# Kernel tuning notes

Measured on AMD Instinct MI355X. Metric: run time of the kernel, lower is better.

Reference implementation:

```python
import jax, jax.numpy as jnp
import numpy as np

N_HEADS = 8
N_DIM = 512
ATTN_DIM = N_DIM // N_HEADS
SOFT_TEMPERATURE = 1.0
TEMPERATURE = ATTN_DIM ** 0.5 / SOFT_TEMPERATURE


def sparsemax(z):
    # sparsemax along last axis: euclidean projection onto the simplex
    n = z.shape[-1]
    z_sorted = -jnp.sort(-z, axis=-1)                      # descending
    cs = jnp.cumsum(z_sorted, axis=-1)
    k = jnp.arange(1, n + 1, dtype=z.dtype)
    support = 1.0 + k * z_sorted > cs                      # bool
    k_sel = jnp.sum(support, axis=-1, keepdims=True)       # support size >= 1
    cs_sel = jnp.take_along_axis(cs, k_sel - 1, axis=-1)
    tau = (cs_sel - 1.0) / k_sel.astype(z.dtype)
    return jnp.maximum(z - tau, 0.0)


def setup_inputs() -> dict:
    key = jax.random.key(0)
    ks = jax.random.split(key, 9)
    bs, L, d = 8, 1024, N_DIM
    s = 1.0 / np.sqrt(d)
    return {
        "h_q": jax.random.normal(ks[0], (bs, L, d), jnp.float32),
        "h_k": jax.random.normal(ks[1], (bs, L, d), jnp.float32),
        "h_v": jax.random.normal(ks[2], (bs, L, d), jnp.float32),
        "Wq": jax.random.normal(ks[3], (d, d), jnp.float32) * s,
        "Wk": jax.random.normal(ks[4], (d, d), jnp.float32) * s,
        "Wv": jax.random.normal(ks[5], (d, d), jnp.float32) * s,
        "bv": jax.random.normal(ks[6], (d,), jnp.float32) * s,
        "Wf": jax.random.normal(ks[7], (d, d), jnp.float32) * s,
        "bf": jax.random.normal(ks[8], (d,), jnp.float32) * s,
    }


def reference(h_q, h_k, h_v, Wq, Wk, Wv, bv, Wf, bf):
    bs, Lq, _ = h_q.shape
    Lk = h_k.shape[1]
    H, D = N_HEADS, ATTN_DIM
    q = (h_q @ Wq.T).reshape(bs, Lq, H, D).transpose(0, 2, 1, 3)   # bhqd
    k = (h_k @ Wk.T).reshape(bs, Lk, H, D).transpose(0, 2, 1, 3)   # bhkd
    v = (h_v @ Wv.T + bv).reshape(bs, Lk, H, D).transpose(0, 2, 1, 3)
    alpha = jnp.einsum('bhqd,bhkd->bhqk', q / TEMPERATURE, k)
    alpha = sparsemax(alpha)
    res = jnp.einsum('bhqk,bhkd->bhqd', alpha, v)
    res = res.transpose(0, 2, 1, 3).reshape(bs, Lq, H * D)
    return res @ Wf.T + bf
```

## Files before the change

kernel.cpp:

```cpp
#include <hip/hip_runtime.h>
#include <hip/hip_bf16.h>
#include <cstdint>
#include <cstddef>

#define BS 8
#define SEQ 1024
#define DMODEL 512
#define NHEADS 8
#define DHEAD 64
#define QBLK 16
#define PPAD 1032

typedef float f32x4 __attribute__((ext_vector_type(4)));
typedef short bf16x8 __attribute__((ext_vector_type(8)));

static __device__ __forceinline__ unsigned short f2bf(float v) {
    __hip_bfloat16 hb = __float2bfloat16(v);
    return *reinterpret_cast<unsigned short*>(&hb);
}

struct CvtJob { const float* s; unsigned short* d; int n4; };

__global__ __launch_bounds__(256) void cvt_many(
    CvtJob j0, CvtJob j1, CvtJob j2, CvtJob j3, CvtJob j4, CvtJob j5, CvtJob j6)
{
    CvtJob j;
    switch (blockIdx.y) {
        case 0: j = j0; break; case 1: j = j1; break; case 2: j = j2; break;
        case 3: j = j3; break; case 4: j = j4; break; case 5: j = j5; break;
        default: j = j6; break;
    }
    for (int i = blockIdx.x * 256 + threadIdx.x; i < j.n4; i += gridDim.x * 256) {
        const float4 f = ((const float4*)j.s)[i];
        uint2 u;
        u.x = (unsigned)f2bf(f.x) | ((unsigned)f2bf(f.y) << 16);
        u.y = (unsigned)f2bf(f.z) | ((unsigned)f2bf(f.w) << 16);
        ((uint2*)j.d)[i] = u;
    }
}

struct GArgs { const unsigned short* A; const unsigned short* W;
               const float* bias; void* C; void* C2; float scale; int mode; };

__global__ __launch_bounds__(256) void gemm_mfma(GArgs g0, GArgs g1, GArgs g2) {
    __shared__ __align__(16) unsigned short As[64 * 64];
    __shared__ __align__(16) unsigned short Bs[128 * 64];

    const GArgs g = (blockIdx.z == 0) ? g0 : ((blockIdx.z == 1) ? g1 : g2);
    const int tid = threadIdx.x;
    const int w = tid >> 6, l = tid & 63, lr = l & 15, lg = l >> 4;
    const int bm = blockIdx.y * 64, bn = blockIdx.x * 128;
    const int mrow = (w & 1) * 32, ncol = (w >> 1) * 64;

    f32x4 acc[2][4];
#pragma unroll
    for (int mt = 0; mt < 2; ++mt)
#pragma unroll
        for (int nt = 0; nt < 4; ++nt) acc[mt][nt] = (f32x4)0.f;

    for (int k0 = 0; k0 < DMODEL; k0 += 64) {
#pragma unroll
        for (int i = 0; i < 2; ++i) {
            const int rbase = i * 32 + w * 8;
            const int r = rbase + (l >> 3);
            const unsigned short* src = g.A + (size_t)(bm + r) * DMODEL + k0
                                        + 8 * ((l & 7) ^ (r & 7));
            __builtin_amdgcn_global_load_lds((const unsigned int*)src,
                                             (unsigned int*)&As[rbase * 64], 16, 0, 0);
        }
#pragma unroll
        for (int i = 0; i < 4; ++i) {
            const int rbase = i * 32 + w * 8;
            const int r = rbase + (l >> 3);
            const unsigned short* src = g.W + (size_t)(bn + r) * DMODEL + k0
                                        + 8 * ((l & 7) ^ (r & 7));
            __builtin_amdgcn_global_load_lds((const unsigned int*)src,
                                             (unsigned int*)&Bs[rbase * 64], 16, 0, 0);
        }
        __syncthreads();
#pragma unroll
        for (int kk = 0; kk < 2; ++kk) {
            bf16x8 av[2], bv[4];
#pragma unroll
            for (int mt = 0; mt < 2; ++mt) {
                const int ra = mrow + mt * 16 + lr;
                av[mt] = *(const bf16x8*)&As[ra * 64 + 8 * ((kk * 4 + lg) ^ (ra & 7))];
            }
#pragma unroll
            for (int nt = 0; nt < 4; ++nt) {
                const int rb = ncol + nt * 16 + lr;
                bv[nt] = *(const bf16x8*)&Bs[rb * 64 + 8 * ((kk * 4 + lg) ^ (rb & 7))];
            }
#pragma unroll
            for (int mt = 0; mt < 2; ++mt)
#pragma unroll
                for (int nt = 0; nt < 4; ++nt)
                    acc[mt][nt] = __builtin_amdgcn_mfma_f32_16x16x32_bf16(
                        av[mt], bv[nt], acc[mt][nt], 0, 0, 0);
        }
        __syncthreads();
    }

    if (g.mode == 0) {
        float* C = (float*)g.C;
#pragma unroll
        for (int mt = 0; mt < 2; ++mt)
#pragma unroll
        for (int nt = 0; nt < 4; ++nt)
#pragma unroll
        for (int j = 0; j < 4; ++j) {
            const int r = bm + mrow + mt * 16 + lg * 4 + j;
            const int c = bn + ncol + nt * 16 + lr;
            C[(size_t)r * DMODEL + c] = acc[mt][nt][j] * g.scale
                                        + (g.bias ? g.bias[c] : 0.f);
        }
    } else {
        if (g.mode == 1 || g.mode == 3) {
            unsigned short* C = (unsigned short*)g.C;
#pragma unroll
            for (int mt = 0; mt < 2; ++mt)
#pragma unroll
            for (int nt = 0; nt < 4; ++nt)
#pragma unroll
            for (int j = 0; j < 4; ++j) {
                const int r = bm + mrow + mt * 16 + lg * 4 + j;
                const int c = bn + ncol + nt * 16 + lr;
                const float v = acc[mt][nt][j] * g.scale + (g.bias ? g.bias[c] : 0.f);
                const int b = r >> 10, ll = r & (SEQ - 1);
                const int h = c >> 6, dd = c & 63;
                C[((size_t)(b * NHEADS + h) * SEQ + ll) * DHEAD + dd] = f2bf(v);
            }
        }
        if (g.mode == 2 || g.mode == 3) {
            unsigned short* C = (unsigned short*)((g.mode == 3) ? g.C2 : g.C);
#pragma unroll
            for (int mt = 0; mt < 2; ++mt)
#pragma unroll
            for (int nt = 0; nt < 4; ++nt) {
                const int c = bn + ncol + nt * 16 + lr;
                const int h = c >> 6, dd = c & 63;
                const int r0 = bm + mrow + mt * 16 + lg * 4;
                const int b = r0 >> 10, l0 = r0 & (SEQ - 1);
                unsigned short tmp[4];
#pragma unroll
                for (int j = 0; j < 4; ++j)
                    tmp[j] = f2bf(acc[mt][nt][j] * g.scale + (g.bias ? g.bias[c] : 0.f));
                uint2 u;
                u.x = (unsigned)tmp[0] | ((unsigned)tmp[1] << 16);
                u.y = (unsigned)tmp[2] | ((unsigned)tmp[3] << 16);
                *(uint2*)&C[((size_t)(b * NHEADS + h) * DHEAD + dd) * SEQ + l0] = u;
            }
        }
    }
}

__global__ __launch_bounds__(256, 3) void attn_mfma(
    const unsigned short* __restrict__ Q, const unsigned short* __restrict__ K,
    const unsigned short* __restrict__ Vt, const unsigned short* __restrict__ Vn,
    unsigned short* __restrict__ R)
{
    __shared__ __align__(16) unsigned char pool[33024];
    __shared__ __align__(16) float clist[QBLK][66];
    __shared__ __align__(16) unsigned short cidx[QBLK][66];
    __shared__ int cnt_s[QBLK];
    __shared__ __align__(16) float red_m[QBLK][4];
    __shared__ __align__(16) float red_s[2][QBLK][4];
    __shared__ __align__(16) float red_c[2][QBLK][4];
    __shared__ float tau_s[QBLK];

    unsigned short* Ks = (unsigned short*)pool;
    unsigned short (*P)[PPAD] = (unsigned short (*)[PPAD])pool;

    const int tid = threadIdx.x;
    const int w = tid >> 6, l = tid & 63, lr = l & 15, lg = l >> 4;

    const int flat = blockIdx.x;
    const int nid = (flat & 7) * 512 + (flat >> 3);
    const int q0 = (nid & 63) * QBLK;
    const int h = (nid >> 6) & (NHEADS - 1);
    const int b = nid >> 9;

    const size_t base = (size_t)(b * NHEADS + h) * SEQ * DHEAD;
    const unsigned short* Qp = Q + base;
    const unsigned short* Kp = K + base;

    const bf16x8 aq0 = *(const bf16x8*)(Qp + (size_t)(q0 + lr) * DHEAD + lg * 8);
    const bf16x8 aq1 = *(const bf16x8*)(Qp + (size_t)(q0 + lr) * DHEAD + 32 + lg * 8);

#define STAGE(CH, BUF)                                                         \
    {                                                                          \
        _Pragma("unroll")                                                      \
        for (int i = 0; i < 4; ++i) {                                          \
            const int rbase = i * 32 + w * 8;                                  \
            const int r = rbase + (l >> 3);                                    \
            const unsigned short* src = Kp + (size_t)((CH) * 128 + r) * DHEAD  \
                                        + 8 * ((l & 7) ^ (r & 7));             \
            __builtin_amdgcn_global_load_lds((const unsigned int*)src,         \
                (unsigned int*)&Ks[(BUF) * 8192 + rbase * 64], 16, 0, 0);      \
        }                                                                      \
    }

    f32x4 acc[16];
#pragma unroll
    for (int a = 0; a < 16; ++a) acc[a] = (f32x4)0.f;

    STAGE(0, 0)
    __syncthreads();
#pragma unroll
    for (int c = 0; c < 8; ++c) {
        const int buf = c & 1;
        if (c + 1 < 8) STAGE(c + 1, buf ^ 1)
        const unsigned short* kb = Ks + buf * 8192;
#pragma unroll
        for (int tt = 0; tt < 2; ++tt) {
            const int ra = w * 32 + tt * 16 + lr;
            const bf16x8 k0 = *(const bf16x8*)&kb[ra * 64 + 8 * ((0 + lg) ^ (ra & 7))];
            const bf16x8 k1 = *(const bf16x8*)&kb[ra * 64 + 8 * ((4 + lg) ^ (ra & 7))];
            acc[2 * c + tt] = __builtin_amdgcn_mfma_f32_16x16x32_bf16(
                k0, aq0, acc[2 * c + tt], 0, 0, 0);
            acc[2 * c + tt] = __builtin_amdgcn_mfma_f32_16x16x32_bf16(
                k1, aq1, acc[2 * c + tt], 0, 0, 0);
        }
        __syncthreads();
    }
#undef STAGE

    f32x4 m4 = acc[0];
#pragma unroll
    for (int a = 1; a < 16; ++a) {
        m4[0] = fmaxf(m4[0], acc[a][0]); m4[1] = fmaxf(m4[1], acc[a][1]);
        m4[2] = fmaxf(m4[2], acc[a][2]); m4[3] = fmaxf(m4[3], acc[a][3]);
    }
    float m = fmaxf(fmaxf(m4[0], m4[1]), fmaxf(m4[2], m4[3]));
    m = fmaxf(m, __shfl_xor(m, 16));
    m = fmaxf(m, __shfl_xor(m, 32));
    if (lg == 0) red_m[lr][w] = m;

    for (int i = tid; i < QBLK * 66; i += 256) (&clist[0][0])[i] = -3.0e38f;
    if (tid < QBLK) cnt_s[tid] = 0;
    __syncthreads();

    const float4 rm4 = *(const float4*)red_m[lr];
    const float rmax = fmaxf(fmaxf(rm4.x, rm4.y), fmaxf(rm4.z, rm4.w));
    float tau = rmax - 1.0f;
    const float thr = tau;

#pragma unroll
    for (int a = 0; a < 16; ++a)
#pragma unroll
        for (int j = 0; j < 4; ++j) {
            const float z = acc[a][j];
            if (z > thr) {
                const int pos = atomicAdd(&cnt_s[lr], 1);
                if (pos < 64) {
                    clist[lr][pos] = z;
                    cidx[lr][pos] = (unsigned short)((a >> 1) * 128 + w * 32
                                                     + (a & 1) * 16 + lg * 4 + j);
                }
            }
        }
    __syncthreads();

    const bool anyfull = __any(cnt_s[lr] > 64);

    if (!anyfull) {
        const f32x4* clp = (const f32x4*)&clist[lr][lg * 16];
        const f32x4 cd0 = clp[0], cd1 = clp[1], cd2 = clp[2], cd3 = clp[3];
        for (int it = 0; it < 16; ++it) {
            float s = 0.f, c = 0.f;
#pragma unroll
            for (int i = 0; i < 4; ++i) {
                const float z0 = cd0[i], z1 = cd1[i], z2 = cd2[i], z3 = cd3[i];
                if (z0 > tau) { s += z0; c += 1.f; }
                if (z1 > tau) { s += z1; c += 1.f; }
                if (z2 > tau) { s += z2; c += 1.f; }
                if (z3 > tau) { s += z3; c += 1.f; }
            }
            s += __shfl_xor(s, 16); c += __shfl_xor(c, 16);
            s += __shfl_xor(s, 32); c += __shfl_xor(c, 32);
            const float tn = (s - 1.f) / c;
            float delta = tn - tau;
            tau = tn;
            delta = fmaxf(delta, __shfl_xor(delta, 1));
            delta = fmaxf(delta, __shfl_xor(delta, 2));
            delta = fmaxf(delta, __shfl_xor(delta, 4));
            delta = fmaxf(delta, __shfl_xor(delta, 8));
            if (delta < 1e-5f) break;
        }
        if (w == 0 && lg == 0) tau_s[lr] = tau;
        __syncthreads();

        const int r = tid >> 4;
        const int dt = tid & 15;
        const float taur = tau_s[r];
        const int cntc = cnt_s[r];
        const unsigned short* Vrow = Vn + base + dt * 4;
        f32x4 o = (f32x4)0.f;
        float z0, z1, z2, z3;
        uint2 v0, v1, v2, v3;
#define SLOAD(ZS, VS, I)                                                       \
    {                                                                          \
        const int ii = (I) < cntc ? (I) : 0;                                   \
        ZS = clist[r][ii];                                                     \
        VS = *(const uint2*)(Vrow + (size_t)cidx[r][ii] * DHEAD);              \
    }
#define SMAC(ZS, VS)                                                           \
    {                                                                          \
        const float wgt = fmaxf(ZS - taur, 0.f);                               \
        o[0] += wgt * __uint_as_float(VS.x << 16);                             \
        o[1] += wgt * __uint_as_float(VS.x & 0xffff0000u);                     \
        o[2] += wgt * __uint_as_float(VS.y << 16);                             \
        o[3] += wgt * __uint_as_float(VS.y & 0xffff0000u);                     \
    }
        SLOAD(z0, v0, 0) SLOAD(z1, v1, 1) SLOAD(z2, v2, 2) SLOAD(z3, v3, 3)
        for (int i = 0; i < cntc; i += 4) {
            SMAC(z0, v0)
            if (i + 1 < cntc) SMAC(z1, v1)
            if (i + 2 < cntc) SMAC(z2, v2)
            if (i + 3 < cntc) SMAC(z3, v3)
            SLOAD(z0, v0, i + 4) SLOAD(z1, v1, i + 5)
            SLOAD(z2, v2, i + 6) SLOAD(z3, v3, i + 7)
        }
#undef SLOAD
#undef SMAC
        unsigned short t4[4];
#pragma unroll
        for (int j = 0; j < 4; ++j) t4[j] = f2bf(o[j]);
        uint2 u;
        u.x = (unsigned)t4[0] | ((unsigned)t4[1] << 16);
        u.y = (unsigned)t4[2] | ((unsigned)t4[3] << 16);
        *(uint2*)&R[((size_t)b * SEQ + q0 + r) * DMODEL + h * DHEAD + dt * 4] = u;
        return;
    }

    for (int it = 0; it < 16; ++it) {
        const int bb = (it + 1) & 1;
        float s = 0.f, c = 0.f;
#pragma unroll
        for (int a = 0; a < 16; ++a)
#pragma unroll
            for (int j = 0; j < 4; ++j) {
                const float z = acc[a][j];
                if (z > tau) { s += z; c += 1.f; }
            }
        s += __shfl_xor(s, 16); c += __shfl_xor(c, 16);
        s += __shfl_xor(s, 32); c += __shfl_xor(c, 32);
        if (lg == 0) { red_s[bb][lr][w] = s; red_c[bb][lr][w] = c; }
        __syncthreads();
        const float4 s4 = *(const float4*)red_s[bb][lr];
        const float4 c4 = *(const float4*)red_c[bb][lr];
        const float st = (s4.x + s4.y) + (s4.z + s4.w);
        const float ct = (c4.x + c4.y) + (c4.z + c4.w);
        const float tn = (st - 1.f) / ct;
        float delta = tn - tau;
        tau = tn;
        delta = fmaxf(delta, __shfl_xor(delta, 1));
        delta = fmaxf(delta, __shfl_xor(delta, 2));
        delta = fmaxf(delta, __shfl_xor(delta, 4));
        delta = fmaxf(delta, __shfl_xor(delta, 8));
        if (delta < 1e-5f) break;
    }
    __syncthreads();

#pragma unroll
    for (int a = 0; a < 16; ++a)
#pragma unroll
        for (int jp = 0; jp < 2; ++jp) {
            const unsigned lo = f2bf(fmaxf(acc[a][2 * jp] - tau, 0.f));
            const unsigned hi = f2bf(fmaxf(acc[a][2 * jp + 1] - tau, 0.f));
            const int key = (a >> 1) * 128 + w * 32 + (a & 1) * 16 + lg * 4 + 2 * jp;
            *(unsigned*)&P[lr][key] = lo | (hi << 16);
        }
    __syncthreads();

    const int dcol = w * 16;
    const unsigned short* VtP = Vt + ((size_t)(b * NHEADS + h) * DHEAD + dcol + lr) * SEQ
                                + lg * 8;
    f32x4 o = (f32x4)0.f;
    bf16x8 vb0 = *(const bf16x8*)(VtP + 0 * 32);
    bf16x8 vb1 = *(const bf16x8*)(VtP + 1 * 32);
    bf16x8 vb2 = *(const bf16x8*)(VtP + 2 * 32);
    bf16x8 vb3 = *(const bf16x8*)(VtP + 3 * 32);
#define PV_STEP(KT, VREG)                                                      \
    {                                                                          \
        const bf16x8 pa = *(const bf16x8*)&P[lr][(KT) * 32 + lg * 8];          \
        o = __builtin_amdgcn_mfma_f32_16x16x32_bf16(pa, VREG, o, 0, 0, 0);     \
        if ((KT) + 4 < 32) VREG = *(const bf16x8*)(VtP + ((KT) + 4) * 32);     \
    }
    for (int kt = 0; kt < 32; kt += 4) {
        PV_STEP(kt + 0, vb0)
        PV_STEP(kt + 1, vb1)
        PV_STEP(kt + 2, vb2)
        PV_STEP(kt + 3, vb3)
    }
#undef PV_STEP

#pragma unroll
    for (int j = 0; j < 4; ++j)
        R[((size_t)b * SEQ + q0 + lg * 4 + j) * DMODEL + h * DHEAD + dcol + lr] =
            f2bf(o[j]);
}

extern "C" void kernel_launch(void* const* d_in, const int* in_sizes, int n_in,
                              void* d_out, int out_size, void* d_ws, size_t ws_size,
                              hipStream_t stream) {
    const float* h_q = (const float*)d_in[0];
    const float* h_k = (const float*)d_in[1];
    const float* h_v = (const float*)d_in[2];
    const float* Wq  = (const float*)d_in[3];
    const float* Wk  = (const float*)d_in[4];
    const float* Wv  = (const float*)d_in[5];
    const float* bv  = (const float*)d_in[6];
    const float* Wf  = (const float*)d_in[7];
    const float* bf  = (const float*)d_in[8];
    float* out = (float*)d_out;

    const size_t perT = (size_t)BS * SEQ * DMODEL;
    const size_t wN = (size_t)DMODEL * DMODEL;
    unsigned short* hq_b = (unsigned short*)d_ws;
    unsigned short* hk_b = hq_b + perT;
    unsigned short* hv_b = hk_b + perT;
    unsigned short* Qws  = hv_b + perT;
    unsigned short* Kws  = Qws + perT;
    unsigned short* Vtw  = Kws + perT;
    unsigned short* Vnw  = Vtw + perT;
    unsigned short* Rws  = Vnw + perT;
    unsigned short* Wqb  = Rws + perT;
    unsigned short* Wkb  = Wqb + wN;
    unsigned short* Wvb  = Wkb + wN;
    unsigned short* Wfb  = Wvb + wN;

    {
        CvtJob j0{h_q, hq_b, (int)(perT / 4)};
        CvtJob j1{h_k, hk_b, (int)(perT / 4)};
        CvtJob j2{h_v, hv_b, (int)(perT / 4)};
        CvtJob j3{Wq, Wqb, (int)(wN / 4)};
        CvtJob j4{Wk, Wkb, (int)(wN / 4)};
        CvtJob j5{Wv, Wvb, (int)(wN / 4)};
        CvtJob j6{Wf, Wfb, (int)(wN / 4)};
        cvt_many<<<dim3(512, 7), 256, 0, stream>>>(j0, j1, j2, j3, j4, j5, j6);
    }

    {
        GArgs gq{hq_b, Wqb, nullptr, Qws, nullptr, 0.125f, 1};
        GArgs gk{hk_b, Wkb, nullptr, Kws, nullptr, 1.0f, 1};
        GArgs gv{hv_b, Wvb, bv,      Vnw, Vtw,     1.0f, 3};
        gemm_mfma<<<dim3(DMODEL / 128, BS * SEQ / 64, 3), 256, 0, stream>>>(gq, gk, gv);
    }

    attn_mfma<<<dim3(BS * NHEADS * (SEQ / QBLK)), 256, 0, stream>>>(Qws, Kws, Vtw, Vnw, Rws);

    {
        GArgs gf{Rws, Wfb, bf, out, nullptr, 1.0f, 0};
        gemm_mfma<<<dim3(DMODEL / 128, BS * SEQ / 64, 1), 256, 0, stream>>>(gf, gf, gf);
    }
}
```

Measured before the change: 169.9 us.

## Process 32 query rows per attention block with 8 waves sharing K tiles

Doubles the query block to 32 rows and the attention block to 512 threads, split into two groups of four waves. Each group handles 16 query rows and both share the same staged K chunks in LDS, halving global K traffic per query. The fallback sparsemax path now runs serially per query group, always runs 16 iterations with two barriers each, and drops the early-exit check. This adds barrier and occupancy cost, and the shared P buffer may not hold 32 rows in the fast path (unclear from the visible code).

```diff
diff --git a/kernel.cpp b/kernel.cpp
--- a/kernel.cpp
+++ b/kernel.cpp
@@ -8,7 +8,7 @@
 #define DMODEL 512
 #define NHEADS 8
 #define DHEAD 64
-#define QBLK 16
+#define QBLK 32
 #define PPAD 1032
 
 typedef float f32x4 __attribute__((ext_vector_type(4)));
@@ -154,7 +154,7 @@
     }
 }
 
-__global__ __launch_bounds__(256, 3) void attn_mfma(
+__global__ __launch_bounds__(512) void attn_mfma(
     const unsigned short* __restrict__ Q, const unsigned short* __restrict__ K,
     const unsigned short* __restrict__ Vt, const unsigned short* __restrict__ Vn,
     unsigned short* __restrict__ R)
@@ -164,8 +164,8 @@
     __shared__ __align__(16) unsigned short cidx[QBLK][66];
     __shared__ int cnt_s[QBLK];
     __shared__ __align__(16) float red_m[QBLK][4];
-    __shared__ __align__(16) float red_s[2][QBLK][4];
-    __shared__ __align__(16) float red_c[2][QBLK][4];
+    __shared__ __align__(16) float red_s[16][4];
+    __shared__ __align__(16) float red_c[16][4];
     __shared__ float tau_s[QBLK];
 
     unsigned short* Ks = (unsigned short*)pool;
@@ -173,25 +173,27 @@
 
     const int tid = threadIdx.x;
     const int w = tid >> 6, l = tid & 63, lr = l & 15, lg = l >> 4;
+    const int wq = w >> 2, wk = w & 3;
 
     const int flat = blockIdx.x;
-    const int nid = (flat & 7) * 512 + (flat >> 3);
-    const int q0 = (nid & 63) * QBLK;
-    const int h = (nid >> 6) & (NHEADS - 1);
-    const int b = nid >> 9;
+    const int nid = (flat & 7) * 256 + (flat >> 3);
+    const int q0 = (nid & 31) * QBLK;
+    const int h = (nid >> 5) & (NHEADS - 1);
+    const int b = nid >> 8;
 
     const size_t base = (size_t)(b * NHEADS + h) * SEQ * DHEAD;
     const unsigned short* Qp = Q + base;
     const unsigned short* Kp = K + base;
 
-    const bf16x8 aq0 = *(const bf16x8*)(Qp + (size_t)(q0 + lr) * DHEAD + lg * 8);
-    const bf16x8 aq1 = *(const bf16x8*)(Qp + (size_t)(q0 + lr) * DHEAD + 32 + lg * 8);
+    const int qrow = q0 + wq * 16 + lr;
+    const bf16x8 aq0 = *(const bf16x8*)(Qp + (size_t)qrow * DHEAD + lg * 8);
+    const bf16x8 aq1 = *(const bf16x8*)(Qp + (size_t)qrow * DHEAD + 32 + lg * 8);
 
 #define STAGE(CH, BUF)                                                         \
     {                                                                          \
         _Pragma("unroll")                                                      \
-        for (int i = 0; i < 4; ++i) {                                          \
-            const int rbase = i * 32 + w * 8;                                  \
+        for (int i = 0; i < 2; ++i) {                                          \
+            const int rbase = i * 64 + w * 8;                                  \
             const int r = rbase + (l >> 3);                                    \
             const unsigned short* src = Kp + (size_t)((CH) * 128 + r) * DHEAD  \
                                         + 8 * ((l & 7) ^ (r & 7));             \
@@ -213,7 +215,7 @@
         const unsigned short* kb = Ks + buf * 8192;
 #pragma unroll
         for (int tt = 0; tt < 2; ++tt) {
-            const int ra = w * 32 + tt * 16 + lr;
+            const int ra = wk * 32 + tt * 16 + lr;
             const bf16x8 k0 = *(const bf16x8*)&kb[ra * 64 + 8 * ((0 + lg) ^ (ra & 7))];
             const bf16x8 k1 = *(const bf16x8*)&kb[ra * 64 + 8 * ((4 + lg) ^ (ra & 7))];
             acc[2 * c + tt] = __builtin_amdgcn_mfma_f32_16x16x32_bf16(
@@ -234,13 +236,13 @@
     float m = fmaxf(fmaxf(m4[0], m4[1]), fmaxf(m4[2], m4[3]));
     m = fmaxf(m, __shfl_xor(m, 16));
     m = fmaxf(m, __shfl_xor(m, 32));
-    if (lg == 0) red_m[lr][w] = m;
-
-    for (int i = tid; i < QBLK * 66; i += 256) (&clist[0][0])[i] = -3.0e38f;
+    if (lg == 0) red_m[wq * 16 + lr][wk] = m;
+
+    for (int i = tid; i < QBLK * 66; i += 512) (&clist[0][0])[i] = -3.0e38f;
     if (tid < QBLK) cnt_s[tid] = 0;
     __syncthreads();
 
-    const float4 rm4 = *(const float4*)red_m[lr];
+    const float4 rm4 = *(const float4*)red_m[wq * 16 + lr];
     const float rmax = fmaxf(fmaxf(rm4.x, rm4.y), fmaxf(rm4.z, rm4.w));
     float tau = rmax - 1.0f;
     const float thr = tau;
@@ -251,20 +253,21 @@
         for (int j = 0; j < 4; ++j) {
             const float z = acc[a][j];
             if (z > thr) {
-                const int pos = atomicAdd(&cnt_s[lr], 1);
+                const int pos = atomicAdd(&cnt_s[wq * 16 + lr], 1);
                 if (pos < 64) {
-                    clist[lr][pos] = z;
-                    cidx[lr][pos] = (unsigned short)((a >> 1) * 128 + w * 32
-                                                     + (a & 1) * 16 + lg * 4 + j);
+                    clist[wq * 16 + lr][pos] = z;
+                    cidx[wq * 16 + lr][pos] = (unsigned short)((a >> 1) * 128 + wk * 32
+                                                               + (a & 1) * 16 + lg * 4 + j);
                 }
             }
         }
     __syncthreads();
 
-    const bool anyfull = __any(cnt_s[lr] > 64);
+    const bool anyfull = __any(cnt_s[l & 31] > 64);
 
     if (!anyfull) {
-        const f32x4* clp = (const f32x4*)&clist[lr][lg * 16];
+        const int R_ = wq * 16 + lr;
+        const f32x4* clp = (const f32x4*)&clist[R_][lg * 16];
         const f32x4 cd0 = clp[0], cd1 = clp[1], cd2 = clp[2], cd3 = clp[3];
         for (int it = 0; it < 16; ++it) {
             float s = 0.f, c = 0.f;
@@ -287,7 +290,7 @@
             delta = fmaxf(delta, __shfl_xor(delta, 8));
             if (delta < 1e-5f) break;
         }
-        if (w == 0 && lg == 0) tau_s[lr] = tau;
+        if (wk == 0 && lg == 0) tau_s[R_] = tau;
         __syncthreads();
 
         const int r = tid >> 4;
@@ -333,72 +336,73 @@
         return;
     }
 
-    for (int it = 0; it < 16; ++it) {
-        const int bb = (it + 1) & 1;
-        float s = 0.f, c = 0.f;
-#pragma unroll
-        for (int a = 0; a < 16; ++a)
-#pragma unroll
-            for (int j = 0; j < 4; ++j) {
-                const float z = acc[a][j];
-                if (z > tau) { s += z; c += 1.f; }
-            }
-        s += __shfl_xor(s, 16); c += __shfl_xor(c, 16);
-        s += __shfl_xor(s, 32); c += __shfl_xor(c, 32);
-        if (lg == 0) { red_s[bb][lr][w] = s; red_c[bb][lr][w] = c; }
-        __syncthreads();
-        const float4 s4 = *(const float4*)red_s[bb][lr];
-        const float4 c4 = *(const float4*)red_c[bb][lr];
-        const float st = (s4.x + s4.y) + (s4.z + s4.w);
-        const float ct = (c4.x + c4.y) + (c4.z + c4.w);
-        const float tn = (st - 1.f) / ct;
-        float delta = tn - tau;
-        tau = tn;
-        delta = fmaxf(delta, __shfl_xor(delta, 1));
-        delta = fmaxf(delta, __shfl_xor(delta, 2));
-        delta = fmaxf(delta, __shfl_xor(delta, 4));
-        delta = fmaxf(delta, __shfl_xor(delta, 8));
-        if (delta < 1e-5f) break;
-    }
-    __syncthreads();
-
-#pragma unroll
-    for (int a = 0; a < 16; ++a)
-#pragma unroll
-        for (int jp = 0; jp < 2; ++jp) {
-            const unsigned lo = f2bf(fmaxf(acc[a][2 * jp] - tau, 0.f));
-            const unsigned hi = f2bf(fmaxf(acc[a][2 * jp + 1] - tau, 0.f));
-            const int key = (a >> 1) * 128 + w * 32 + (a & 1) * 16 + lg * 4 + 2 * jp;
-            *(unsigned*)&P[lr][key] = lo | (hi << 16);
-        }
-    __syncthreads();
-
-    const int dcol = w * 16;
-    const unsigned short* VtP = Vt + ((size_t)(b * NHEADS + h) * DHEAD + dcol + lr) * SEQ
-                                + lg * 8;
-    f32x4 o = (f32x4)0.f;
-    bf16x8 vb0 = *(const bf16x8*)(VtP + 0 * 32);
-    bf16x8 vb1 = *(const bf16x8*)(VtP + 1 * 32);
-    bf16x8 vb2 = *(const bf16x8*)(VtP + 2 * 32);
-    bf16x8 vb3 = *(const bf16x8*)(VtP + 3 * 32);
+    for (int qg = 0; qg < 2; ++qg) {
+        const bool act = (wq == qg);
+        for (int it = 0; it < 16; ++it) {
+            float s = 0.f, c = 0.f;
+            if (act) {
+#pragma unroll
+                for (int a = 0; a < 16; ++a)
+#pragma unroll
+                    for (int j = 0; j < 4; ++j) {
+                        const float z = acc[a][j];
+                        if (z > tau) { s += z; c += 1.f; }
+                    }
+                s += __shfl_xor(s, 16); c += __shfl_xor(c, 16);
+                s += __shfl_xor(s, 32); c += __shfl_xor(c, 32);
+                if (lg == 0) { red_s[lr][wk] = s; red_c[lr][wk] = c; }
+            }
+            __syncthreads();
+            if (act) {
+                const float4 s4 = *(const float4*)red_s[lr];
+                const float4 c4 = *(const float4*)red_c[lr];
+                const float st = (s4.x + s4.y) + (s4.z + s4.w);
+                const float ct = (c4.x + c4.y) + (c4.z + c4.w);
+                tau = (st - 1.f) / ct;
+            }
+            __syncthreads();
+        }
+        if (act) {
+#pragma unroll
+            for (int a = 0; a < 16; ++a)
+#pragma unroll
+                for (int jp = 0; jp < 2; ++jp) {
+                    const unsigned lo = f2bf(fmaxf(acc[a][2 * jp] - tau, 0.f));
+                    const unsigned hi = f2bf(fmaxf(acc[a][2 * jp + 1] - tau, 0.f));
+                    const int key = (a >> 1) * 128 + wk * 32 + (a & 1) * 16 + lg * 4 + 2 * jp;
+                    *(unsigned*)&P[lr][key] = lo | (hi << 16);
+                }
+        }
+        __syncthreads();
+        if (act) {
+            const int dcol = wk * 16;
+            const unsigned short* VtP = Vt + ((size_t)(b * NHEADS + h) * DHEAD + dcol + lr)
+                                        * SEQ + lg * 8;
+            f32x4 o = (f32x4)0.f;
+            bf16x8 vb0 = *(const bf16x8*)(VtP + 0 * 32);
+            bf16x8 vb1 = *(const bf16x8*)(VtP + 1 * 32);
+            bf16x8 vb2 = *(const bf16x8*)(VtP + 2 * 32);
+            bf16x8 vb3 = *(const bf16x8*)(VtP + 3 * 32);
 #define PV_STEP(KT, VREG)                                                      \
     {                                                                          \
         const bf16x8 pa = *(const bf16x8*)&P[lr][(KT) * 32 + lg * 8];          \
         o = __builtin_amdgcn_mfma_f32_16x16x32_bf16(pa, VREG, o, 0, 0, 0);     \
         if ((KT) + 4 < 32) VREG = *(const bf16x8*)(VtP + ((KT) + 4) * 32);     \
     }
-    for (int kt = 0; kt < 32; kt += 4) {
-        PV_STEP(kt + 0, vb0)
-        PV_STEP(kt + 1, vb1)
-        PV_STEP(kt + 2, vb2)
-        PV_STEP(kt + 3, vb3)
-    }
+            for (int kt = 0; kt < 32; kt += 4) {
+                PV_STEP(kt + 0, vb0)
+                PV_STEP(kt + 1, vb1)
+                PV_STEP(kt + 2, vb2)
+                PV_STEP(kt + 3, vb3)
+            }
 #undef PV_STEP
-
-#pragma unroll
-    for (int j = 0; j < 4; ++j)
-        R[((size_t)b * SEQ + q0 + lg * 4 + j) * DMODEL + h * DHEAD + dcol + lr] =
-            f2bf(o[j]);
+#pragma unroll
+            for (int j = 0; j < 4; ++j)
+                R[((size_t)b * SEQ + q0 + qg * 16 + lg * 4 + j) * DMODEL
+                  + h * DHEAD + dcol + lr] = f2bf(o[j]);
+        }
+        __syncthreads();
+    }
 }
 
 extern "C" void kernel_launch(void* const* d_in, const int* in_sizes, int n_in,
@@ -448,7 +452,7 @@
         gemm_mfma<<<dim3(DMODEL / 128, BS * SEQ / 64, 3), 256, 0, stream>>>(gq, gk, gv);
     }
 
-    attn_mfma<<<dim3(BS * NHEADS * (SEQ / QBLK)), 256, 0, stream>>>(Qws, Kws, Vtw, Vnw, Rws);
+    attn_mfma<<<dim3(BS * NHEADS * (SEQ / QBLK)), 512, 0, stream>>>(Qws, Kws, Vtw, Vnw, Rws);
 
     {
         GArgs gf{Rws, Wfb, bf, out, nullptr, 1.0f, 0};
```

Measured after the change: 235.6 us. +38.6%, slower.

## Shrink attention LDS footprint to raise occupancy via segmented P staging

Applied to the files above, without the earlier changes.

Drops K double-buffering so it uses a single 16KB buffer, and replaces the full 16x1024 bf16 probability tile in LDS with a per-segment 16x128 tile that is written and consumed in eight steps. Launch bounds go from 3 to 6 blocks per CU to use the freed LDS for higher occupancy. The trade-off is losing the overlap between K loads and MFMA, adding extra barriers per PV segment, and dropping the V register prefetch pipeline. There is also more register pressure at the higher occupancy target.

```diff
diff --git a/kernel.cpp b/kernel.cpp
--- a/kernel.cpp
+++ b/kernel.cpp
@@ -9,7 +9,6 @@
 #define NHEADS 8
 #define DHEAD 64
 #define QBLK 16
-#define PPAD 1032
 
 typedef float f32x4 __attribute__((ext_vector_type(4)));
 typedef short bf16x8 __attribute__((ext_vector_type(8)));
@@ -154,22 +153,23 @@
     }
 }
 
-__global__ __launch_bounds__(256, 3) void attn_mfma(
+__global__ __launch_bounds__(256, 6) void attn_mfma(
     const unsigned short* __restrict__ Q, const unsigned short* __restrict__ K,
     const unsigned short* __restrict__ Vt, const unsigned short* __restrict__ Vn,
     unsigned short* __restrict__ R)
 {
-    __shared__ __align__(16) unsigned char pool[33024];
-    __shared__ __align__(16) float clist[QBLK][66];
-    __shared__ __align__(16) unsigned short cidx[QBLK][66];
+    __shared__ __align__(16) unsigned short Ks[128 * 64];
+    __shared__ __align__(16) unsigned char spool[6400];
     __shared__ int cnt_s[QBLK];
     __shared__ __align__(16) float red_m[QBLK][4];
     __shared__ __align__(16) float red_s[2][QBLK][4];
     __shared__ __align__(16) float red_c[2][QBLK][4];
     __shared__ float tau_s[QBLK];
 
-    unsigned short* Ks = (unsigned short*)pool;
-    unsigned short (*P)[PPAD] = (unsigned short (*)[PPAD])pool;
+    float (*clist)[66] = (float (*)[66])spool;
+    unsigned short (*cidx)[66] =
+        (unsigned short (*)[66])(spool + 4224);
+    unsigned short* Pseg = (unsigned short*)spool;
 
     const int tid = threadIdx.x;
     const int w = tid >> 6, l = tid & 63, lr = l & 15, lg = l >> 4;
@@ -187,7 +187,7 @@
     const bf16x8 aq0 = *(const bf16x8*)(Qp + (size_t)(q0 + lr) * DHEAD + lg * 8);
     const bf16x8 aq1 = *(const bf16x8*)(Qp + (size_t)(q0 + lr) * DHEAD + 32 + lg * 8);
 
-#define STAGE(CH, BUF)                                                         \
+#define STAGE(CH)                                                              \
     {                                                                          \
         _Pragma("unroll")                                                      \
         for (int i = 0; i < 4; ++i) {                                          \
@@ -196,7 +196,7 @@
             const unsigned short* src = Kp + (size_t)((CH) * 128 + r) * DHEAD  \
                                         + 8 * ((l & 7) ^ (r & 7));             \
             __builtin_amdgcn_global_load_lds((const unsigned int*)src,         \
-                (unsigned int*)&Ks[(BUF) * 8192 + rbase * 64], 16, 0, 0);      \
+                (unsigned int*)&Ks[rbase * 64], 16, 0, 0);                     \
         }                                                                      \
     }
 
@@ -204,18 +204,15 @@
 #pragma unroll
     for (int a = 0; a < 16; ++a) acc[a] = (f32x4)0.f;
 
-    STAGE(0, 0)
-    __syncthreads();
 #pragma unroll
     for (int c = 0; c < 8; ++c) {
-        const int buf = c & 1;
-        if (c + 1 < 8) STAGE(c + 1, buf ^ 1)
-        const unsigned short* kb = Ks + buf * 8192;
+        STAGE(c)
+        __syncthreads();
 #pragma unroll
         for (int tt = 0; tt < 2; ++tt) {
             const int ra = w * 32 + tt * 16 + lr;
-            const bf16x8 k0 = *(const bf16x8*)&kb[ra * 64 + 8 * ((0 + lg) ^ (ra & 7))];
-            const bf16x8 k1 = *(const bf16x8*)&kb[ra * 64 + 8 * ((4 + lg) ^ (ra & 7))];
+            const bf16x8 k0 = *(const bf16x8*)&Ks[ra * 64 + 8 * ((0 + lg) ^ (ra & 7))];
+            const bf16x8 k1 = *(const bf16x8*)&Ks[ra * 64 + 8 * ((4 + lg) ^ (ra & 7))];
             acc[2 * c + tt] = __builtin_amdgcn_mfma_f32_16x16x32_bf16(
                 k0, aq0, acc[2 * c + tt], 0, 0, 0);
             acc[2 * c + tt] = __builtin_amdgcn_mfma_f32_16x16x32_bf16(
@@ -362,43 +359,37 @@
     }
     __syncthreads();
 
-#pragma unroll
-    for (int a = 0; a < 16; ++a)
-#pragma unroll
-        for (int jp = 0; jp < 2; ++jp) {
-            const unsigned lo = f2bf(fmaxf(acc[a][2 * jp] - tau, 0.f));
-            const unsigned hi = f2bf(fmaxf(acc[a][2 * jp + 1] - tau, 0.f));
-            const int key = (a >> 1) * 128 + w * 32 + (a & 1) * 16 + lg * 4 + 2 * jp;
-            *(unsigned*)&P[lr][key] = lo | (hi << 16);
-        }
-    __syncthreads();
-
-    const int dcol = w * 16;
-    const unsigned short* VtP = Vt + ((size_t)(b * NHEADS + h) * DHEAD + dcol + lr) * SEQ
-                                + lg * 8;
-    f32x4 o = (f32x4)0.f;
-    bf16x8 vb0 = *(const bf16x8*)(VtP + 0 * 32);
-    bf16x8 vb1 = *(const bf16x8*)(VtP + 1 * 32);
-    bf16x8 vb2 = *(const bf16x8*)(VtP + 2 * 32);
-    bf16x8 vb3 = *(const bf16x8*)(VtP + 3 * 32);
-#define PV_STEP(KT, VREG)                                                      \
-    {                                                                          \
-        const bf16x8 pa = *(const bf16x8*)&P[lr][(KT) * 32 + lg * 8];          \
-        o = __builtin_amdgcn_mfma_f32_16x16x32_bf16(pa, VREG, o, 0, 0, 0);     \
-        if ((KT) + 4 < 32) VREG = *(const bf16x8*)(VtP + ((KT) + 4) * 32);     \
-    }
-    for (int kt = 0; kt < 32; kt += 4) {
-        PV_STEP(kt + 0, vb0)
-        PV_STEP(kt + 1, vb1)
-        PV_STEP(kt + 2, vb2)
-        PV_STEP(kt + 3, vb3)
-    }
-#undef PV_STEP
-
-#pragma unroll
-    for (int j = 0; j < 4; ++j)
-        R[((size_t)b * SEQ + q0 + lg * 4 + j) * DMODEL + h * DHEAD + dcol + lr] =
-            f2bf(o[j]);
+    {
+        const int dcol = w * 16;
+        const unsigned short* VtP = Vt + ((size_t)(b * NHEADS + h) * DHEAD + dcol + lr)
+                                    * SEQ + lg * 8;
+        f32x4 o = (f32x4)0.f;
+        for (int seg = 0; seg < 8; ++seg) {
+#pragma unroll
+            for (int tt = 0; tt < 2; ++tt) {
+                const int a = 2 * seg + tt;
+#pragma unroll
+                for (int jp = 0; jp < 2; ++jp) {
+                    const unsigned lo = f2bf(fmaxf(acc[a][2 * jp] - tau, 0.f));
+                    const unsigned hi = f2bf(fmaxf(acc[a][2 * jp + 1] - tau, 0.f));
+                    *(unsigned*)&Pseg[lr * 136 + w * 32 + tt * 16 + lg * 4 + 2 * jp] =
+                        lo | (hi << 16);
+                }
+            }
+            __syncthreads();
+#pragma unroll
+            for (int kt = 0; kt < 4; ++kt) {
+                const bf16x8 pa = *(const bf16x8*)&Pseg[lr * 136 + kt * 32 + lg * 8];
+                const bf16x8 vb = *(const bf16x8*)(VtP + seg * 128 + kt * 32);
+                o = __builtin_amdgcn_mfma_f32_16x16x32_bf16(pa, vb, o, 0, 0, 0);
+            }
+            __syncthreads();
+        }
+#pragma unroll
+        for (int j = 0; j < 4; ++j)
+            R[((size_t)b * SEQ + q0 + lg * 4 + j) * DMODEL + h * DHEAD + dcol + lr] =
+                f2bf(o[j]);
+    }
 }
 
 extern "C" void kernel_launch(void* const* d_in, const int* in_sizes, int n_in,
```

Result: slower. 180.9 us (+6.4%).
